# Kernel tuning notes

Hardware: AMD Instinct MI355X
Metric: run time of the kernel (lower is better)

Reference implementation:

```python
import jax, jax.numpy as jnp
import numpy as np

D, H, DH, L, F, NM = 512, 8, 64, 8, 2048, 80
B, S = 8, 1024


def _ln(x, g, b, eps=1e-5):
    mu = x.mean(-1, keepdims=True)
    var = ((x - mu) ** 2).mean(-1, keepdims=True)
    return (x - mu) / jnp.sqrt(var + eps) * g + b


def setup_inputs() -> dict:
    key = jax.random.key(0)
    ks = jax.random.split(key, 16)
    n = lambda k, sh: jax.random.normal(k, sh, dtype=jnp.float32) * 0.02
    # sinusoidal positional encoding, as in PositionalEncoding
    pos = np.arange(S, dtype=np.float32)[:, None]
    div = np.exp(np.arange(0, D, 2, dtype=np.float32) * (-np.log(10000.0) / D))
    pe = np.zeros((S, D), dtype=np.float32)
    pe[:, 0::2] = np.sin(pos * div)
    pe[:, 1::2] = np.cos(pos * div)
    return dict(
        mel=jax.random.normal(ks[0], (B, S, NM), dtype=jnp.float32),
        pe=jnp.asarray(pe),
        proj_w=n(ks[1], (NM, D)), proj_b=jnp.zeros((D,), jnp.float32),
        Wq=n(ks[2], (L, D, D)), bq=jnp.zeros((L, D), jnp.float32),
        Wk=n(ks[3], (L, D, D)), bk=jnp.zeros((L, D), jnp.float32),
        Wv=n(ks[4], (L, D, D)), bv=jnp.zeros((L, D), jnp.float32),
        Wo=n(ks[5], (L, D, D)), bo=jnp.zeros((L, D), jnp.float32),
        ln1_g=jnp.ones((L, D), jnp.float32), ln1_b=jnp.zeros((L, D), jnp.float32),
        ln2_g=jnp.ones((L, D), jnp.float32), ln2_b=jnp.zeros((L, D), jnp.float32),
        Wi=n(ks[6], (L, D, F)), bi=jnp.zeros((L, F), jnp.float32),
        Wf=n(ks[7], (L, F, D)), bf=jnp.zeros((L, D), jnp.float32),
        lnf_g=jnp.ones((D,), jnp.float32), lnf_b=jnp.zeros((D,), jnp.float32),
        lang_w=n(ks[8], (D, 100)), lang_b=jnp.zeros((100,), jnp.float32),
        int_w=n(ks[9], (D, 50)), int_b=jnp.zeros((50,), jnp.float32),
        emo_w=n(ks[10], (D, 8)), emo_b=jnp.zeros((8,), jnp.float32),
        sp_w=n(ks[11], (D, 1000)), sp_b=jnp.zeros((1000,), jnp.float32),
    )


def reference(mel, pe, proj_w, proj_b, Wq, bq, Wk, bk, Wv, bv, Wo, bo,
              ln1_g, ln1_b, ln2_g, ln2_b, Wi, bi, Wf, bf,
              lnf_g, lnf_b, lang_w, lang_b, int_w, int_b, emo_w, emo_b, sp_w, sp_b):
    # feature extraction projection + positional encoding
    h = mel @ proj_w + proj_b + pe[None]  # (B, S, D)
    scale = 1.0 / np.sqrt(DH)

    def block(h, p):
        wq, bq_, wk, bk_, wv, bv_, wo, bo_, g1, b1, g2, b2, wi, bi_, wf, bf_ = p
        x = _ln(h, g1, b1)
        b, s, _ = x.shape
        heads = lambda y, w, bias: (y @ w + bias).reshape(b, s, H, DH).transpose(0, 2, 1, 3)
        q, k, v = heads(x, wq, bq_), heads(x, wk, bk_), heads(x, wv, bv_)
        probs = jax.nn.softmax(jnp.einsum('bhqd,bhkd->bhqk', q, k) * scale, axis=-1)
        ctx = jnp.einsum('bhqk,bhkd->bhqd', probs, v).transpose(0, 2, 1, 3).reshape(b, s, D)
        h = h + ctx @ wo + bo_
        y = _ln(h, g2, b2)
        h = h + jax.nn.gelu(y @ wi + bi_, approximate=False) @ wf + bf_
        return h, None

    h, _ = jax.lax.scan(block, h, (Wq, bq, Wk, bk, Wv, bv, Wo, bo,
                                   ln1_g, ln1_b, ln2_g, ln2_b, Wi, bi, Wf, bf))
    h = _ln(h, lnf_g, lnf_b)
    pooled = h.mean(axis=1)  # no mask: sequence_lengths=None path
    language_logits = pooled @ lang_w + lang_b
    intent_logits = pooled @ int_w + int_b
    emotion_logits = pooled @ emo_w + emo_b
    speech_logits = h @ sp_w + sp_b
    return (language_logits, intent_logits, emotion_logits, speech_logits)
```

## Files before the change

### kernel.cpp

```cpp
#include <hip/hip_runtime.h>
#include <hip/hip_bf16.h>
#include <math.h>

#define DD   512
#define HH   8
#define DHH  64
#define LL   8
#define FF   2048
#define NMEL 80
#define BB   8
#define SS   1024
#define MM   (BB*SS)

typedef __attribute__((ext_vector_type(8))) short bf16x8;
typedef __attribute__((ext_vector_type(4))) float f32x4;
typedef __attribute__((ext_vector_type(4))) unsigned short u16x4;
typedef __attribute__((ext_vector_type(8))) unsigned short u16x8;

#define GLOAD_LDS16(g, l) __builtin_amdgcn_global_load_lds( \
    (const __attribute__((address_space(1))) void*)(g),      \
    (__attribute__((address_space(3))) void*)(l), 16, 0, 0)

__device__ __forceinline__ unsigned short f2bf(float x) {
    __hip_bfloat16 b = __float2bfloat16(x);
    return *reinterpret_cast<unsigned short*>(&b);
}

__global__ __launch_bounds__(256) void proj_pe_kernel(
    const float* __restrict__ mel, const float* __restrict__ pw,
    const float* __restrict__ pb, const float* __restrict__ pe,
    float* __restrict__ h)
{
    int row = blockIdx.x;
    int s = row & (SS - 1);
    __shared__ float m_s[NMEL];
    int t = threadIdx.x;
    if (t < NMEL) m_s[t] = mel[(size_t)row * NMEL + t];
    __syncthreads();
    for (int d = t; d < DD; d += 256) {
        float acc = pb[d] + pe[(size_t)s * DD + d];
        #pragma unroll 8
        for (int k = 0; k < NMEL; ++k)
            acc = fmaf(m_s[k], pw[(size_t)k * DD + d], acc);
        h[(size_t)row * DD + d] = acc;
    }
}

__global__ __launch_bounds__(512) void ln_kernel(
    const float* __restrict__ in, const float* __restrict__ g,
    const float* __restrict__ bta, __hip_bfloat16* __restrict__ out)
{
    int w = threadIdx.x >> 6, lane = threadIdx.x & 63;
    int row = blockIdx.x * 8 + w;
    const float4* xr = reinterpret_cast<const float4*>(in + (size_t)row * DD) + lane * 2;
    float4 v0 = xr[0], v1 = xr[1];
    float s  = v0.x + v0.y + v0.z + v0.w + v1.x + v1.y + v1.z + v1.w;
    float ss = v0.x*v0.x + v0.y*v0.y + v0.z*v0.z + v0.w*v0.w
             + v1.x*v1.x + v1.y*v1.y + v1.z*v1.z + v1.w*v1.w;
    #pragma unroll
    for (int off = 1; off < 64; off <<= 1) {
        s  += __shfl_xor(s, off);
        ss += __shfl_xor(ss, off);
    }
    float mu  = s * (1.f / DD);
    float var = ss * (1.f / DD) - mu * mu;
    float rstd = rsqrtf(var + 1e-5f);
    const float4* gp = reinterpret_cast<const float4*>(g) + lane * 2;
    const float4* bp = reinterpret_cast<const float4*>(bta) + lane * 2;
    float4 g0 = gp[0], g1 = gp[1], b0 = bp[0], b1 = bp[1];
    u16x8 o;
    o[0] = f2bf((v0.x - mu) * rstd * g0.x + b0.x);
    o[1] = f2bf((v0.y - mu) * rstd * g0.y + b0.y);
    o[2] = f2bf((v0.z - mu) * rstd * g0.z + b0.z);
    o[3] = f2bf((v0.w - mu) * rstd * g0.w + b0.w);
    o[4] = f2bf((v1.x - mu) * rstd * g1.x + b1.x);
    o[5] = f2bf((v1.y - mu) * rstd * g1.y + b1.y);
    o[6] = f2bf((v1.z - mu) * rstd * g1.z + b1.z);
    o[7] = f2bf((v1.w - mu) * rstd * g1.w + b1.w);
    *reinterpret_cast<u16x8*>(out + (size_t)row * DD + lane * 8) = o;
}

__global__ __launch_bounds__(256) void wconv_kernel(
    const float* __restrict__ in, __hip_bfloat16* __restrict__ out,
    int K, int N, int rstride, int rowoff)
{
    __shared__ float tile[32][33];
    size_t lin  = (size_t)blockIdx.z * K * N;
    size_t lout = (size_t)blockIdx.z * rstride * K + (size_t)rowoff * K;
    int tx = threadIdx.x & 31, ty = threadIdx.x >> 5;
    int n0 = blockIdx.x * 32, k0 = blockIdx.y * 32;
    #pragma unroll
    for (int i = 0; i < 32; i += 8) {
        int k = k0 + ty + i, n = n0 + tx;
        tile[ty + i][tx] = (n < N) ? in[lin + (size_t)k * N + n] : 0.f;
    }
    __syncthreads();
    #pragma unroll
    for (int i = 0; i < 32; i += 8) {
        int n = n0 + ty + i, k = k0 + tx;
        out[lout + (size_t)n * K + k] = __float2bfloat16(tile[tx][ty + i]);
    }
}

template<int BN, int OUTMODE, bool GELU_EP, bool RESID>
__global__ __launch_bounds__(512) void gemm_bf16(
    const __hip_bfloat16* __restrict__ A,
    const __hip_bfloat16* __restrict__ Bt,
    const float* __restrict__ b0, const float* __restrict__ b1,
    const float* __restrict__ b2,
    const float* __restrict__ resid,
    float* __restrict__ Cf,
    __hip_bfloat16* __restrict__ O0, __hip_bfloat16* __restrict__ O1,
    __hip_bfloat16* __restrict__ O2,
    int M, int N, int K)
{
    constexpr int MI = (BN == 128) ? 4 : 2;
    constexpr int NI = 2;
    __shared__ __align__(16) __hip_bfloat16 As[128 * 64];
    __shared__ __align__(16) __hip_bfloat16 Bs[BN * 64];
    int t = threadIdx.x;
    int w = t >> 6, lane = t & 63, g = lane >> 4, li = lane & 15;
    int wm = (BN == 128) ? (w >> 2) : (w >> 1);
    int wn = (BN == 128) ? (w & 3) : (w & 1);

    int nwg = gridDim.x * gridDim.y;
    int linb = blockIdx.y * gridDim.x + blockIdx.x;
    int xcd = linb & 7, idx = linb >> 3;
    int q8 = nwg >> 3, r8 = nwg & 7;
    int swz = (xcd < r8 ? xcd * (q8 + 1) : r8 * (q8 + 1) + (xcd - r8) * q8) + idx;
    size_t bm = (size_t)(swz / gridDim.x) * 128;
    size_t bn = (size_t)(swz % gridDim.x) * BN;

    const f32x4 vzero = {0.f, 0.f, 0.f, 0.f};
    f32x4 acc[MI][NI];
    #pragma unroll
    for (int i = 0; i < MI; ++i)
        #pragma unroll
        for (int j = 0; j < NI; ++j) acc[i][j] = vzero;

    for (int k0 = 0; k0 < K; k0 += 64) {
        #pragma unroll
        for (int i = 0; i < 2; ++i) {
            int c = i * 512 + t;
            int row = c >> 3, col = (c & 7) << 3;
            GLOAD_LDS16(A + (bm + row) * (size_t)K + k0 + col, As + (size_t)c * 8);
        }
        #pragma unroll
        for (int i = 0; i < BN / 64; ++i) {
            int c = i * 512 + t;
            int row = c >> 3, col = (c & 7) << 3;
            GLOAD_LDS16(Bt + (bn + row) * (size_t)K + k0 + col, Bs + (size_t)c * 8);
        }
        __syncthreads();
        #pragma unroll
        for (int kk = 0; kk < 2; ++kk) {
            bf16x8 af[MI], bfr[NI];
            #pragma unroll
            for (int mi = 0; mi < MI; ++mi)
                af[mi] = *reinterpret_cast<const bf16x8*>(As + (wm * (MI * 16) + mi * 16 + li) * 64 + kk * 32 + g * 8);
            #pragma unroll
            for (int ni = 0; ni < NI; ++ni)
                bfr[ni] = *reinterpret_cast<const bf16x8*>(Bs + (wn * 32 + ni * 16 + li) * 64 + kk * 32 + g * 8);
            #pragma unroll
            for (int mi = 0; mi < MI; ++mi)
                #pragma unroll
                for (int ni = 0; ni < NI; ++ni)
                    acc[mi][ni] = __builtin_amdgcn_mfma_f32_16x16x32_bf16(af[mi], bfr[ni], acc[mi][ni], 0, 0, 0);
        }
        __syncthreads();
    }

    #pragma unroll
    for (int mi = 0; mi < MI; ++mi) {
        #pragma unroll
        for (int ni = 0; ni < NI; ++ni) {
            f32x4 v = acc[mi][ni];
            int coll = wn * 32 + ni * 16 + li;
            size_t col = bn + coll;
            if ((int)col >= N) continue;
            float bv;
            int sel = 0, c = (int)col;
            if (OUTMODE == 2) {
                sel = (int)(col >> 9); c = (int)(col & 511);
                bv = (sel == 0) ? b0[c] : (sel == 1) ? b1[c] : b2[c];
            } else {
                bv = b0[col];
            }
            #pragma unroll
            for (int r = 0; r < 4; ++r) {
                size_t row = bm + wm * (MI * 16) + mi * 16 + g * 4 + r;
                float x = v[r] + bv;
                if (GELU_EP) x = 0.5f * x * (1.f + erff(x * 0.70710678118654752440f));
                if (RESID)   x += resid[row * (size_t)N + col];
                if (OUTMODE == 0) {
                    Cf[row * (size_t)N + col] = x;
                } else if (OUTMODE == 1) {
                    O0[row * (size_t)N + col] = __float2bfloat16(x);
                } else {
                    size_t b = row >> 10, s = row & (SS - 1);
                    size_t h = (size_t)(c >> 6), d = (size_t)(c & 63);
                    __hip_bfloat16 xb = __float2bfloat16(x);
                    if (sel == 0)      O0[((b * HH + h) << 16) + (s << 6) + d] = xb;
                    else if (sel == 1) O1[((b * HH + h) << 16) + (s << 6) + d] = xb;
                    else               O2[((b * HH + h) << 16) + (d << 10) + s] = xb;
                }
            }
        }
    }
}

__global__ __launch_bounds__(512, 4) void attn_mfma(
    const __hip_bfloat16* __restrict__ qb,
    const __hip_bfloat16* __restrict__ kb,
    const __hip_bfloat16* __restrict__ vtb,
    __hip_bfloat16* __restrict__ ctx)
{
    __shared__ __align__(16) char smem[49152];
    unsigned short (*Plds)[32][40] = (unsigned short (*)[32][40])smem;
    float* comb = (float*)smem;

    int t = threadIdx.x;
    int w = t >> 6, lane = t & 63, g = lane >> 4, li = lane & 15;
    int wq = w & 3, wk = w >> 2;
    int bh = blockIdx.x;
    int b = bh >> 3, h = bh & 7;
    int q0 = blockIdx.y * 128 + wq * 32;

    const __hip_bfloat16* Qp = qb  + ((size_t)bh << 16);
    const __hip_bfloat16* Kp = kb  + ((size_t)bh << 16);
    const __hip_bfloat16* Vp = vtb + ((size_t)bh << 16);

    bf16x8 qf[2][2];
    #pragma unroll
    for (int qt = 0; qt < 2; ++qt)
        #pragma unroll
        for (int kk = 0; kk < 2; ++kk)
            qf[qt][kk] = *reinterpret_cast<const bf16x8*>(
                Qp + (size_t)(q0 + qt * 16 + li) * DHH + kk * 32 + g * 8);

    const f32x4 vzero = {0.f, 0.f, 0.f, 0.f};
    f32x4 acc_oT[2][4];
    float m_r[2], l_r[2];
    #pragma unroll
    for (int qt = 0; qt < 2; ++qt) {
        #pragma unroll
        for (int dt = 0; dt < 4; ++dt) acc_oT[qt][dt] = vzero;
        m_r[qt] = -1e30f; l_r[qt] = 0.f;
    }

    const float csc = 0.125f * 1.44269504088896340736f;

    #pragma unroll 2
    for (int it = 0; it < 16; ++it) {
        int ks0 = wk * 512 + it * 32;
        f32x4 accs[2][2];
        #pragma unroll
        for (int qt = 0; qt < 2; ++qt)
            #pragma unroll
            for (int kt = 0; kt < 2; ++kt) accs[qt][kt] = vzero;
        #pragma unroll
        for (int kk = 0; kk < 2; ++kk) {
            bf16x8 kf[2];
            #pragma unroll
            for (int kt = 0; kt < 2; ++kt)
                kf[kt] = *reinterpret_cast<const bf16x8*>(
                    Kp + (size_t)(ks0 + kt * 16 + li) * DHH + kk * 32 + g * 8);
            #pragma unroll
            for (int qt = 0; qt < 2; ++qt)
                #pragma unroll
                for (int kt = 0; kt < 2; ++kt)
                    accs[qt][kt] = __builtin_amdgcn_mfma_f32_16x16x32_bf16(kf[kt], qf[qt][kk], accs[qt][kt], 0, 0, 0);
        }

        bf16x8 vf[4];
        #pragma unroll
        for (int dt = 0; dt < 4; ++dt)
            vf[dt] = *reinterpret_cast<const bf16x8*>(
                Vp + (size_t)(dt * 16 + li) * SS + ks0 + g * 8);

        float mnew[2];
        #pragma unroll
        for (int qt = 0; qt < 2; ++qt) {
            float a0 = fmaxf(fmaxf(accs[qt][0][0], accs[qt][0][1]),
                             fmaxf(accs[qt][0][2], accs[qt][0][3]));
            float a1 = fmaxf(fmaxf(accs[qt][1][0], accs[qt][1][1]),
                             fmaxf(accs[qt][1][2], accs[qt][1][3]));
            float m = fmaxf(a0, a1);
            m = fmaxf(m, __shfl_xor(m, 16));
            m = fmaxf(m, __shfl_xor(m, 32));
            mnew[qt] = m * csc;
        }

        bool grow = (mnew[0] > m_r[0] + 11.0f) || (mnew[1] > m_r[1] + 11.0f);
        if (__any(grow)) {
            #pragma unroll
            for (int qt = 0; qt < 2; ++qt) {
                float mn = fmaxf(m_r[qt], mnew[qt]);
                float alpha = exp2f(m_r[qt] - mn);
                m_r[qt] = mn;
                l_r[qt] *= alpha;
                #pragma unroll
                for (int dt = 0; dt < 4; ++dt)
                    #pragma unroll
                    for (int r = 0; r < 4; ++r)
                        acc_oT[qt][dt][r] *= alpha;
            }
        }

        float rs[2] = {0.f, 0.f};
        #pragma unroll
        for (int qt = 0; qt < 2; ++qt) {
            #pragma unroll
            for (int kt = 0; kt < 2; ++kt) {
                u16x4 pk;
                #pragma unroll
                for (int r = 0; r < 4; ++r) {
                    float p = exp2f(fmaf(accs[qt][kt][r], csc, -m_r[qt]));
                    rs[qt] += p;
                    pk[r] = f2bf(p);
                }
                *reinterpret_cast<u16x4*>(&Plds[w][qt * 16 + li][kt * 16 + g * 4]) = pk;
            }
            float s = rs[qt];
            s += __shfl_xor(s, 16);
            s += __shfl_xor(s, 32);
            l_r[qt] += s;
        }

        bf16x8 pf[2];
        #pragma unroll
        for (int qt = 0; qt < 2; ++qt)
            pf[qt] = *reinterpret_cast<const bf16x8*>(&Plds[w][qt * 16 + li][g * 8]);
        #pragma unroll
        for (int dt = 0; dt < 4; ++dt)
            #pragma unroll
            for (int qt = 0; qt < 2; ++qt)
                acc_oT[qt][dt] = __builtin_amdgcn_mfma_f32_16x16x32_bf16(vf[dt], pf[qt], acc_oT[qt][dt], 0, 0, 0);
    }

    __syncthreads();
    if (wk == 1) {
        float* cb = comb + ((size_t)(w - 4) * 64 + lane) * 36;
        #pragma unroll
        for (int qt = 0; qt < 2; ++qt)
            #pragma unroll
            for (int dt = 0; dt < 4; ++dt)
                *reinterpret_cast<f32x4*>(cb + qt * 16 + dt * 4) = acc_oT[qt][dt];
        #pragma unroll
        for (int qt = 0; qt < 2; ++qt) {
            cb[32 + qt] = m_r[qt];
            cb[34 + qt] = l_r[qt];
        }
    }
    __syncthreads();
    if (wk == 0) {
        float* cb = comb + ((size_t)w * 64 + lane) * 36;
        #pragma unroll
        for (int qt = 0; qt < 2; ++qt) {
            float m2 = cb[32 + qt];
            float l2 = cb[34 + qt];
            float mg = fmaxf(m_r[qt], m2);
            float a1 = exp2f(m_r[qt] - mg);
            float a2 = exp2f(m2 - mg);
            float inv = 1.f / (l_r[qt] * a1 + l2 * a2);
            int q = q0 + qt * 16 + li;
            #pragma unroll
            for (int dt = 0; dt < 4; ++dt) {
                f32x4 ob = *reinterpret_cast<const f32x4*>(cb + qt * 16 + dt * 4);
                u16x4 pk;
                #pragma unroll
                for (int r = 0; r < 4; ++r)
                    pk[r] = f2bf((acc_oT[qt][dt][r] * a1 + ob[r] * a2) * inv);
                *reinterpret_cast<u16x4*>(
                    &ctx[((size_t)(b * SS + q)) * DD + h * DHH + dt * 16 + g * 4]) = pk;
            }
        }
    }
}

__global__ __launch_bounds__(512) void pool_kernel(
    const __hip_bfloat16* __restrict__ hf, float* __restrict__ part)
{
    int b = blockIdx.x >> 5, chunk = blockIdx.x & 31;
    int d = threadIdx.x;
    float acc = 0.f;
    int s0 = chunk * 32;
    for (int s = s0; s < s0 + 32; ++s)
        acc += __bfloat162float(hf[((size_t)(b * SS + s)) * DD + d]);
    part[(size_t)blockIdx.x * DD + d] = acc;
}

__global__ __launch_bounds__(256) void heads_kernel(
    const float* __restrict__ part,
    const float* __restrict__ lw, const float* __restrict__ lb,
    const float* __restrict__ iw, const float* __restrict__ ib,
    const float* __restrict__ ew, const float* __restrict__ eb,
    float* __restrict__ out)
{
    int b = blockIdx.x;
    __shared__ float ps[DD];
    int t = threadIdx.x;
    float a0 = 0.f, a1 = 0.f;
    for (int c = 0; c < 32; ++c) {
        const float* p = part + ((size_t)(b * 32 + c)) * DD;
        a0 += p[t];
        a1 += p[t + 256];
    }
    ps[t]       = a0 * (1.f / SS);
    ps[t + 256] = a1 * (1.f / SS);
    __syncthreads();
    if (t < 158) {
        const float* wptr; const float* bptr; float* optr; int n; int j;
        if (t < 100)      { j = t;       wptr = lw; bptr = lb; optr = out;        n = 100; }
        else if (t < 150) { j = t - 100; wptr = iw; bptr = ib; optr = out + 800;  n = 50;  }
        else              { j = t - 150; wptr = ew; bptr = eb; optr = out + 1200; n = 8;   }
        float acc = bptr[j];
        for (int k2 = 0; k2 < DD; ++k2)
            acc = fmaf(ps[k2], wptr[(size_t)k2 * n + j], acc);
        optr[b * n + j] = acc;
    }
}

extern "C" void kernel_launch(void* const* d_in, const int* in_sizes, int n_in,
                              void* d_out, int out_size, void* d_ws, size_t ws_size,
                              hipStream_t stream)
{
    const float* mel    = (const float*)d_in[0];
    const float* pe     = (const float*)d_in[1];
    const float* proj_w = (const float*)d_in[2];
    const float* proj_b = (const float*)d_in[3];
    const float* Wq     = (const float*)d_in[4];
    const float* bq     = (const float*)d_in[5];
    const float* Wk     = (const float*)d_in[6];
    const float* bk     = (const float*)d_in[7];
    const float* Wv     = (const float*)d_in[8];
    const float* bv     = (const float*)d_in[9];
    const float* Wo     = (const float*)d_in[10];
    const float* bo     = (const float*)d_in[11];
    const float* ln1_g  = (const float*)d_in[12];
    const float* ln1_b  = (const float*)d_in[13];
    const float* ln2_g  = (const float*)d_in[14];
    const float* ln2_b  = (const float*)d_in[15];
    const float* Wi     = (const float*)d_in[16];
    const float* bi     = (const float*)d_in[17];
    const float* Wf     = (const float*)d_in[18];
    const float* bf     = (const float*)d_in[19];
    const float* lnf_g  = (const float*)d_in[20];
    const float* lnf_b  = (const float*)d_in[21];
    const float* lang_w = (const float*)d_in[22];
    const float* lang_b = (const float*)d_in[23];
    const float* int_w  = (const float*)d_in[24];
    const float* int_b  = (const float*)d_in[25];
    const float* emo_w  = (const float*)d_in[26];
    const float* emo_b  = (const float*)d_in[27];
    const float* sp_w   = (const float*)d_in[28];
    const float* sp_b   = (const float*)d_in[29];

    float* out = (float*)d_out;
    char* wsb = (char*)d_ws;

    const size_t MB = 1ull << 20;
    float* hbuf           = (float*)(wsb);
    __hip_bfloat16* xb    = (__hip_bfloat16*)(wsb + 16 * MB);
    __hip_bfloat16* qbuf  = (__hip_bfloat16*)(wsb + 24 * MB);
    __hip_bfloat16* kbuf  = (__hip_bfloat16*)(wsb + 32 * MB);
    __hip_bfloat16* vtb   = (__hip_bfloat16*)(wsb + 40 * MB);
    __hip_bfloat16* ctx   = (__hip_bfloat16*)(wsb + 48 * MB);
    __hip_bfloat16* gbuf  = (__hip_bfloat16*)(wsb + 24 * MB);
    float* part           = (float*)(wsb + 56 * MB);
    __hip_bfloat16* wqkv  = (__hip_bfloat16*)(wsb + 57 * MB);
    __hip_bfloat16* wot   = (__hip_bfloat16*)(wsb + 70 * MB);
    __hip_bfloat16* wit   = (__hip_bfloat16*)(wsb + 74 * MB);
    __hip_bfloat16* wft   = (__hip_bfloat16*)(wsb + 90 * MB);
    __hip_bfloat16* spt   = (__hip_bfloat16*)(wsb + 107 * MB);

    wconv_kernel<<<dim3(16, 16, LL), 256, 0, stream>>>(Wq, wqkv, DD, DD, 1536, 0);
    wconv_kernel<<<dim3(16, 16, LL), 256, 0, stream>>>(Wk, wqkv, DD, DD, 1536, 512);
    wconv_kernel<<<dim3(16, 16, LL), 256, 0, stream>>>(Wv, wqkv, DD, DD, 1536, 1024);
    wconv_kernel<<<dim3(16, 16, LL), 256, 0, stream>>>(Wo, wot, DD, DD, DD, 0);
    wconv_kernel<<<dim3(64, 16, LL), 256, 0, stream>>>(Wi, wit, DD, FF, FF, 0);
    wconv_kernel<<<dim3(16, 64, LL), 256, 0, stream>>>(Wf, wft, FF, DD, DD, 0);
    wconv_kernel<<<dim3(32, 16, 1),  256, 0, stream>>>(sp_w, spt, DD, 1000, 1024, 0);

    proj_pe_kernel<<<MM, 256, 0, stream>>>(mel, proj_w, proj_b, pe, hbuf);

    for (int l = 0; l < LL; ++l) {
        const __hip_bfloat16* wqkv_l = wqkv + (size_t)l * 1536 * DD;
        const __hip_bfloat16* wot_l  = wot  + (size_t)l * DD * DD;
        const __hip_bfloat16* wit_l  = wit  + (size_t)l * FF * DD;
        const __hip_bfloat16* wft_l  = wft  + (size_t)l * DD * FF;

        ln_kernel<<<MM / 8, 512, 0, stream>>>(hbuf, ln1_g + l * DD, ln1_b + l * DD, xb);

        gemm_bf16<128, 2, false, false><<<dim3(12, 64), 512, 0, stream>>>(
            xb, wqkv_l, bq + l * DD, bk + l * DD, bv + l * DD,
            nullptr, nullptr, qbuf, kbuf, vtb, MM, 1536, DD);

        attn_mfma<<<dim3(BB * HH, SS / 128), 512, 0, stream>>>(qbuf, kbuf, vtb, ctx);

        gemm_bf16<64, 0, false, true><<<dim3(8, 64), 512, 0, stream>>>(
            ctx, wot_l, bo + l * DD, nullptr, nullptr,
            hbuf, hbuf, nullptr, nullptr, nullptr, MM, DD, DD);

        ln_kernel<<<MM / 8, 512, 0, stream>>>(hbuf, ln2_g + l * DD, ln2_b + l * DD, xb);

        gemm_bf16<128, 1, true, false><<<dim3(16, 64), 512, 0, stream>>>(
            xb, wit_l, bi + l * FF, nullptr, nullptr,
            nullptr, nullptr, gbuf, nullptr, nullptr, MM, FF, DD);
        gemm_bf16<64, 0, false, true><<<dim3(8, 64), 512, 0, stream>>>(
            gbuf, wft_l, bf + l * DD, nullptr, nullptr,
            hbuf, hbuf, nullptr, nullptr, nullptr, MM, DD, FF);
    }

    ln_kernel<<<MM / 8, 512, 0, stream>>>(hbuf, lnf_g, lnf_b, xb);
    pool_kernel<<<BB * 32, 512, 0, stream>>>(xb, part);
    heads_kernel<<<BB, 256, 0, stream>>>(part, lang_w, lang_b, int_w, int_b,
                                         emo_w, emo_b, out);

    gemm_bf16<128, 0, false, false><<<dim3(8, 64), 512, 0, stream>>>(
        xb, spt, sp_b, nullptr, nullptr,
        nullptr, out + 1264, nullptr, nullptr, nullptr, MM, 1000, DD);
}
```

Before: 1.701 ms.

## Double-buffer LDS tiles in bf16 GEMM to overlap global loads with MFMA

Converts the GEMM main loop to a two-stage LDS double buffer, so the next K-tile is fetched with global_load_lds while MFMAs run on the current tile. This targets the exposed load latency and the extra barrier of the single-buffered loop. For BN=128 the K-tile shrinks to 32 to keep LDS usage bounded, which halves the work per barrier. The loop relies on the single barrier per iteration to cover completion of the async LDS loads, which may not guarantee the prefetched data is ready.

```diff
diff --git a/kernel.cpp b/kernel.cpp
--- a/kernel.cpp
+++ b/kernel.cpp
@@ -116,8 +116,13 @@
 {
     constexpr int MI = (BN == 128) ? 4 : 2;
     constexpr int NI = 2;
-    __shared__ __align__(16) __hip_bfloat16 As[128 * 64];
-    __shared__ __align__(16) __hip_bfloat16 Bs[BN * 64];
+    constexpr int BK = (BN == 128) ? 32 : 64;
+    constexpr int NKK = BK / 32;
+    constexpr int CPR = BK / 8;
+    constexpr int ALD = 128 * CPR / 512;
+    constexpr int BLD = BN * CPR / 512;
+    __shared__ __align__(16) __hip_bfloat16 As[2][128 * BK];
+    __shared__ __align__(16) __hip_bfloat16 Bs[2][BN * BK];
     int t = threadIdx.x;
     int w = t >> 6, lane = t & 63, g = lane >> 4, li = lane & 15;
     int wm = (BN == 128) ? (w >> 2) : (w >> 1);
@@ -138,29 +143,40 @@
         #pragma unroll
         for (int j = 0; j < NI; ++j) acc[i][j] = vzero;
 
-    for (int k0 = 0; k0 < K; k0 += 64) {
-        #pragma unroll
-        for (int i = 0; i < 2; ++i) {
+    auto stage = [&](int buf, int k0) {
+        #pragma unroll
+        for (int i = 0; i < ALD; ++i) {
             int c = i * 512 + t;
-            int row = c >> 3, col = (c & 7) << 3;
-            GLOAD_LDS16(A + (bm + row) * (size_t)K + k0 + col, As + (size_t)c * 8);
-        }
-        #pragma unroll
-        for (int i = 0; i < BN / 64; ++i) {
+            int row = c / CPR, col = (c % CPR) * 8;
+            GLOAD_LDS16(A + (bm + row) * (size_t)K + k0 + col,
+                        &As[buf][(size_t)c * 8]);
+        }
+        #pragma unroll
+        for (int i = 0; i < BLD; ++i) {
             int c = i * 512 + t;
-            int row = c >> 3, col = (c & 7) << 3;
-            GLOAD_LDS16(Bt + (bn + row) * (size_t)K + k0 + col, Bs + (size_t)c * 8);
-        }
-        __syncthreads();
-        #pragma unroll
-        for (int kk = 0; kk < 2; ++kk) {
+            int row = c / CPR, col = (c % CPR) * 8;
+            GLOAD_LDS16(Bt + (bn + row) * (size_t)K + k0 + col,
+                        &Bs[buf][(size_t)c * 8]);
+        }
+    };
+
+    int nt = K / BK;
+    stage(0, 0);
+    __syncthreads();
+    int cur = 0;
+    for (int kt = 0; kt < nt; ++kt) {
+        if (kt + 1 < nt) stage(cur ^ 1, (kt + 1) * BK);
+        #pragma unroll
+        for (int kk = 0; kk < NKK; ++kk) {
             bf16x8 af[MI], bfr[NI];
             #pragma unroll
             for (int mi = 0; mi < MI; ++mi)
-                af[mi] = *reinterpret_cast<const bf16x8*>(As + (wm * (MI * 16) + mi * 16 + li) * 64 + kk * 32 + g * 8);
+                af[mi] = *reinterpret_cast<const bf16x8*>(
+                    &As[cur][(wm * (MI * 16) + mi * 16 + li) * BK + kk * 32 + g * 8]);
             #pragma unroll
             for (int ni = 0; ni < NI; ++ni)
-                bfr[ni] = *reinterpret_cast<const bf16x8*>(Bs + (wn * 32 + ni * 16 + li) * 64 + kk * 32 + g * 8);
+                bfr[ni] = *reinterpret_cast<const bf16x8*>(
+                    &Bs[cur][(wn * 32 + ni * 16 + li) * BK + kk * 32 + g * 8]);
             #pragma unroll
             for (int mi = 0; mi < MI; ++mi)
                 #pragma unroll
@@ -168,6 +184,7 @@
                     acc[mi][ni] = __builtin_amdgcn_mfma_f32_16x16x32_bf16(af[mi], bfr[ni], acc[mi][ni], 0, 0, 0);
         }
         __syncthreads();
+        cur ^= 1;
     }
 
     #pragma unroll
```

Result: faster. 1.578 ms (-7.2%).
